# Optimization experiments

Measured on AMD Instinct MI355X. Metric: run time of the kernel, lower is better.

Reference implementation:

```python
import jax, jax.numpy as jnp
import numpy as np

B, C, T, H = 256, 8, 1024, 512
WB_INC = 0.05  # task_data_generator.wb_inc


def setup_inputs() -> dict:
    key = jax.random.key(0)
    ks = jax.random.split(key, 8)
    # arms/time strictly positive to keep the likelihood division well-conditioned
    inputs = jax.random.uniform(ks[0], (B, C, T), dtype=jnp.float32) + 0.5
    w_in = jax.random.normal(ks[1], (H, 6), dtype=jnp.float32) / np.sqrt(6.0).astype(np.float32)
    b_in = jax.random.normal(ks[2], (H,), dtype=jnp.float32) * 0.01
    w_rec = jax.random.normal(ks[3], (H, H), dtype=jnp.float32) / np.sqrt(float(H)).astype(np.float32)
    b_rec = jax.random.normal(ks[4], (H,), dtype=jnp.float32) * 0.01
    w_key = jax.random.normal(ks[5], (2, H), dtype=jnp.float32) / np.sqrt(float(H)).astype(np.float32)
    b_key = jax.random.normal(ks[6], (2,), dtype=jnp.float32) * 0.01
    # pre-drawn standard normals for the data-dependent noise injection (one per batch per step)
    z = jax.random.normal(ks[7], (T - 1, B), dtype=jnp.float32)
    return {"inputs": inputs, "w_in": w_in, "b_in": b_in, "w_rec": w_rec,
            "b_rec": b_rec, "w_key": w_key, "b_key": b_key, "z": z}


def _likelihood(tm, arms):
    # ((tm - arm) / (0.15*arm))^2, zeroed where tm == 0
    prs = ((tm[:, None] - arms) / (0.15 * arms)) ** 2
    return jnp.where(tm[:, None] == 0.0, 0.0, prs)


def _forward(inputs, w_in, b_in, w_rec, b_rec, w_key, b_key, z):
    Bsz, _, Tn = inputs.shape
    Hn = w_rec.shape[0]
    in_arms = inputs[:, :6, :]
    tm1 = inputs[:, 6, :]  # (B, T), never modified
    tm2 = inputs[:, 7, :]  # (B, T), receives cumulative noise offsets
    idx_tm1 = jnp.argmax(tm1, axis=1)          # (B,)
    ts = jnp.arange(1, Tn)
    tm1_done = ts[:, None] > idx_tm1[None, :]  # (T-1, B)
    arms_pri = jnp.moveaxis(in_arms[:, :2, 1:], 2, 0)  # (T-1, B, 2)
    arms_sec = jnp.moveaxis(in_arms[:, 2:, 1:], 2, 0)  # (T-1, B, 4)
    tm1_seq = tm1[:, 1:].T                              # (T-1, B)
    tm2_seq = tm2[:, 1:].T                              # (T-1, B)

    def step(carry, xs):
        h_pre, key_h_pre, side_h_pre, offset = carry
        ap, asec, t1, t2o, done, zt = xs
        side_h = key_h_pre > 0.5
        arms_sum = asec[:, :2] * key_h_pre[:, None] + asec[:, 2:] * (1.0 - key_h_pre)[:, None]
        closer1 = jnp.argmin(jnp.abs(ap - t1[:, None]), axis=1) == 0
        away = side_h != closer1
        switched = (side_h != side_h_pre) & done & away
        # in-place suffix update in_time[b,1,t:] += N(0, |wb_inc*tm2_t|) == cumulative per-batch offset
        t2_cur = t2o + offset
        offset = offset + jnp.where(switched, zt * jnp.abs(WB_INC * t2_cur), 0.0)
        t2_eff = t2o + offset
        pr1 = _likelihood(t1, ap)
        pr2 = _likelihood(t2_eff, arms_sum)
        prs_t = jnp.concatenate([pr1, pr2], axis=1)          # (B, 4)
        inp_t = jnp.concatenate([ap, arms_sum, t1[:, None], t2_eff[:, None]], axis=1)  # (B, 6)
        h_t = jnp.tanh(inp_t @ w_in.T + b_in + h_pre @ w_rec.T + b_rec)
        key_t = jax.nn.sigmoid(h_t @ w_key.T + b_key)        # (B, 2)
        return (h_t, key_t[:, 0], side_h, offset), (h_t, prs_t, key_t, t2_eff)

    carry0 = (jnp.zeros((Bsz, Hn), dtype=inputs.dtype),
              jnp.ones((Bsz,), dtype=inputs.dtype),
              jnp.ones((Bsz,), dtype=bool),
              jnp.zeros((Bsz,), dtype=inputs.dtype))
    _, (hs_s, prs_s, keys_s, tm2_s) = jax.lax.scan(
        step, carry0, (arms_pri, arms_sec, tm1_seq, tm2_seq, tm1_done, z))
    # loop starts at t=1; t=0 slots stay zero
    hs = jnp.concatenate([jnp.zeros((Bsz, Hn, 1), dtype=inputs.dtype), jnp.moveaxis(hs_s, 0, 2)], axis=2)
    prs = jnp.concatenate([jnp.zeros((Bsz, 4, 1), dtype=inputs.dtype), jnp.moveaxis(prs_s, 0, 2)], axis=2)
    keys = jnp.concatenate([jnp.zeros((Bsz, 2, 1), dtype=inputs.dtype), jnp.moveaxis(keys_s, 0, 2)], axis=2)
    tm2_mod = jnp.concatenate([tm2[:, :1], tm2_s.T], axis=1)
    tm_modified = jnp.stack([tm1, tm2_mod], axis=1)  # (B, 2, T)
    return keys, prs, hs, tm_modified


def reference(inputs, w_in, b_in, w_rec, b_rec, w_key, b_key, z):
    return _forward(inputs, w_in, b_in, w_rec, b_rec, w_key, b_key, z)
```

## Files before the change

kernel.cpp:

```cpp
#include <hip/hip_runtime.h>
#include <math.h>

#define TN 1024
#define HH 512
#define BB 256
#define NTHR 512
#define NW48 48
#define TSTRIDE 136

#define OFF_KEYS 0L
#define OFF_PRS  524288L
#define OFF_HS   1572864L
#define OFF_TM   135790592L

typedef float f32x4 __attribute__((ext_vector_type(4)));
typedef _Float16 f16x2 __attribute__((ext_vector_type(2)));

__device__ __forceinline__ float sigm(float x) { return 1.0f / (1.0f + expf(-x)); }

__device__ __forceinline__ float dot2(unsigned a, unsigned b, float c) {
#if __has_builtin(__builtin_amdgcn_fdot2)
    return __builtin_amdgcn_fdot2(__builtin_bit_cast(f16x2, a),
                                  __builtin_bit_cast(f16x2, b), c, false);
#else
    const f16x2 x = __builtin_bit_cast(f16x2, a);
    const f16x2 y = __builtin_bit_cast(f16x2, b);
    return fmaf((float)x.y, (float)y.y, fmaf((float)x.x, (float)y.x, c));
#endif
}

__global__ __launch_bounds__(256) void conv_fp16(const float* __restrict__ w,
                                                 _Float16* __restrict__ o) {
    const int i = (blockIdx.x * 256 + threadIdx.x) * 4;
    const f32x4 v = *(const f32x4*)(w + i);
    _Float16 r[4];
    #pragma unroll
    for (int k = 0; k < 4; ++k) r[k] = (_Float16)v[k];
    *(unsigned long long*)(o + i) = *(const unsigned long long*)r;
}

__global__ __launch_bounds__(NTHR, 2) void rnn_fused(
    const float* __restrict__ in, const float* __restrict__ w_in,
    const float* __restrict__ b_in, const float* __restrict__ b_rec,
    const float* __restrict__ w_key, const float* __restrict__ b_key,
    const float* __restrict__ z, float* __restrict__ out,
    const _Float16* __restrict__ whf)
{
    __shared__ __align__(16) _Float16 wtail[HH][TSTRIDE];
    __shared__ __align__(16) float tbuf[HH][9];
    __shared__ __align__(16) _Float16 hsh[2][HH];
    __shared__ float keysT[2][2][16];
    __shared__ float prsT[2][4][16];
    __shared__ float tmT[2][16];
    __shared__ float inp6[8];
    __shared__ float kred[8][2];

    const int tid = threadIdx.x;
    const int bb  = blockIdx.x;
    const int wv  = tid >> 6, ln = tid & 63;
    const float* inb = in + (long)bb * 8 * TN;
    const unsigned* wrow = (const unsigned*)(whf + (long)tid * HH);

    uint4 wreg[NW48];
    #pragma unroll
    for (int i = 0; i < NW48; ++i) wreg[i] = *(const uint4*)(wrow + i * 4);
    {
        const uint4* src = (const uint4*)(wrow + 192);
        #pragma unroll
        for (int i = 0; i < 16; ++i) *(uint4*)&wtail[tid][i * 8] = src[i];
    }

    const float bs  = b_in[tid] + b_rec[tid];
    const float wk0 = w_key[tid], wk1 = w_key[HH + tid];
    const float* wip = w_in + tid * 6;
    const float wi0 = wip[0], wi1 = wip[1], wi2 = wip[2];
    const float wi3 = wip[3], wi4 = wip[4], wi5 = wip[5];

    hsh[0][tid] = (_Float16)0.0f;
    tbuf[tid][0] = 0.0f;
    if (tid < 256) {
        f32x4 v = *(const f32x4*)(inb + 6 * TN + tid * 4);
        __builtin_nontemporal_store(v, (f32x4*)(out + OFF_TM + (long)bb * 2 * TN + tid * 4));
    }
    if (tid == 0) {
        keysT[0][0][0] = 0.f; keysT[0][1][0] = 0.f;
        prsT[0][0][0] = 0.f; prsT[0][1][0] = 0.f;
        prsT[0][2][0] = 0.f; prsT[0][3][0] = 0.f;
        tmT[0][0] = inb[7 * TN];
    }
    int idxm = 0;
    if (wv == 0) {
        const float* tp = inb + 6 * TN;
        float bv = -3.0e38f; int bi = 0;
        for (int i = 0; i < 16; ++i) { int tt = i * 64 + ln; float v = tp[tt]; if (v > bv) { bv = v; bi = tt; } }
        #pragma unroll
        for (int m = 1; m < 64; m <<= 1) {
            float ov = __shfl_xor(bv, m); int oi = __shfl_xor(bi, m);
            if (ov > bv || (ov == bv && oi < bi)) { bv = ov; bi = oi; }
        }
        idxm = bi;
    }
    float kh = 1.0f, off = 0.0f; int side_pre = 1;
    float q0=0,q1=0,q2=0,q3=0,q4=0,q5=0,q6=0,q7=0,qz=0;
    const float bk0 = b_key[0], bk1 = b_key[1];
    if (tid == 0) {
        q0=inb[1]; q1=inb[TN+1]; q2=inb[2*TN+1]; q3=inb[3*TN+1];
        q4=inb[4*TN+1]; q5=inb[5*TN+1]; q6=inb[6*TN+1]; q7=inb[7*TN+1];
        qz=z[bb];
    }
    __syncthreads();

    for (int t = 1; t < TN; ++t) {
        const int par1 = (t - 1) & 1, par2 = t & 1;
        const int tile = (t >> 4) & 1, sl = t & 15;

        if (tid == 0) {
            if (t > 1) {
                float k0 = 0.f, k1 = 0.f;
                #pragma unroll
                for (int w = 0; w < 8; ++w) { k0 += kred[w][0]; k1 += kred[w][1]; }
                const float key0 = sigm(k0 + bk0), key1 = sigm(k1 + bk1);
                const int pt = t - 1;
                keysT[(pt >> 4) & 1][0][pt & 15] = key0;
                keysT[(pt >> 4) & 1][1][pt & 15] = key1;
                kh = key0;
            }
            const int side = (kh > 0.5f);
            const float as0 = q2 * kh + q4 * (1.0f - kh);
            const float as1 = q3 * kh + q5 * (1.0f - kh);
            const int closer1 = (fabsf(q0 - q6) <= fabsf(q1 - q6));
            const int done = (t > idxm);
            const int sw = ((side != side_pre) && done && (side != closer1));
            const float t2c = q7 + off;
            if (sw) off += qz * fabsf(0.05f * t2c);
            const float t2e = q7 + off;
            side_pre = side;
            float u0 = (q6 - q0) / (0.15f * q0);    float pr10 = (q6 == 0.f) ? 0.f : u0 * u0;
            float u1 = (q6 - q1) / (0.15f * q1);    float pr11 = (q6 == 0.f) ? 0.f : u1 * u1;
            float u2 = (t2e - as0) / (0.15f * as0); float pr20 = (t2e == 0.f) ? 0.f : u2 * u2;
            float u3 = (t2e - as1) / (0.15f * as1); float pr21 = (t2e == 0.f) ? 0.f : u3 * u3;
            prsT[tile][0][sl] = pr10; prsT[tile][1][sl] = pr11;
            prsT[tile][2][sl] = pr20; prsT[tile][3][sl] = pr21;
            tmT[tile][sl] = t2e;
            inp6[0] = q0; inp6[1] = q1; inp6[2] = as0;
            inp6[3] = as1; inp6[4] = q6; inp6[5] = t2e;
            const int tn = (t < TN - 1) ? t + 1 : t;
            q0 = inb[tn]; q1 = inb[TN + tn]; q2 = inb[2 * TN + tn]; q3 = inb[3 * TN + tn];
            q4 = inb[4 * TN + tn]; q5 = inb[5 * TN + tn]; q6 = inb[6 * TN + tn]; q7 = inb[7 * TN + tn];
            qz = z[(long)(tn - 1) * BB + bb];
        }

        float a0 = 0.f, a1 = 0.f, a2 = 0.f, a3 = 0.f;
        const unsigned* hb = (const unsigned*)&hsh[par1][0];
        #pragma unroll
        for (int i = 0; i < NW48; ++i) {
            const uint4 hu = *(const uint4*)(hb + i * 4);
            a0 = dot2(wreg[i].x, hu.x, a0);
            a1 = dot2(wreg[i].y, hu.y, a1);
            a2 = dot2(wreg[i].z, hu.z, a2);
            a3 = dot2(wreg[i].w, hu.w, a3);
        }
        #pragma unroll
        for (int i = 0; i < 16; ++i) {
            const uint4 hu = *(const uint4*)(hb + 192 + i * 4);
            const uint4 wu = *(const uint4*)&wtail[tid][i * 8];
            a0 = dot2(wu.x, hu.x, a0);
            a1 = dot2(wu.y, hu.y, a1);
            a2 = dot2(wu.z, hu.z, a2);
            a3 = dot2(wu.w, hu.w, a3);
        }
        const float sdot = (a0 + a1) + (a2 + a3);
        __syncthreads();

        {
            const float s = sdot + bs
                          + wi0 * inp6[0] + wi1 * inp6[1] + wi2 * inp6[2]
                          + wi3 * inp6[3] + wi4 * inp6[4] + wi5 * inp6[5];
            const float h = tanhf(s);
            hsh[par2][tid] = (_Float16)h;
            tbuf[tid][t & 7] = h;
            float ka0 = h * wk0, ka1 = h * wk1;
            #pragma unroll
            for (int m = 1; m < 64; m <<= 1) { ka0 += __shfl_xor(ka0, m); ka1 += __shfl_xor(ka1, m); }
            if (ln == 0) { kred[wv][0] = ka0; kred[wv][1] = ka1; }
        }
        __syncthreads();

        if ((t & 7) == 7) {
            const int t0 = t - 7;
            const float* tr = &tbuf[tid][0];
            f32x4 v0, v1;
            v0.x = tr[0]; v0.y = tr[1]; v0.z = tr[2]; v0.w = tr[3];
            v1.x = tr[4]; v1.y = tr[5]; v1.z = tr[6]; v1.w = tr[7];
            float* dst = out + OFF_HS + ((long)bb * HH + tid) * TN + t0;
            __builtin_nontemporal_store(v0, (f32x4*)dst);
            __builtin_nontemporal_store(v1, (f32x4*)(dst + 4));
        }
        if ((t & 15) == 0 && wv == 0) {
            const int f = tile ^ 1, t0 = t - 16;
            if (ln < 8) {
                const int ch = ln >> 2, c4 = ln & 3;
                __builtin_nontemporal_store(*(const f32x4*)&keysT[f][ch][c4 * 4],
                    (f32x4*)(out + OFF_KEYS + (long)bb * 2 * TN + ch * TN + t0 + c4 * 4));
            } else if (ln < 24) {
                const int ix = ln - 8, ch = ix >> 2, c4 = ix & 3;
                __builtin_nontemporal_store(*(const f32x4*)&prsT[f][ch][c4 * 4],
                    (f32x4*)(out + OFF_PRS + (long)bb * 4 * TN + ch * TN + t0 + c4 * 4));
            } else if (ln < 28) {
                const int c4 = ln - 24;
                __builtin_nontemporal_store(*(const f32x4*)&tmT[f][c4 * 4],
                    (f32x4*)(out + OFF_TM + (long)bb * 2 * TN + TN + t0 + c4 * 4));
            }
        }
    }

    if (tid == 0) {
        float k0 = 0.f, k1 = 0.f;
        #pragma unroll
        for (int w = 0; w < 8; ++w) { k0 += kred[w][0]; k1 += kred[w][1]; }
        keysT[1][0][15] = sigm(k0 + bk0);
        keysT[1][1][15] = sigm(k1 + bk1);
    }
    __syncthreads();
    if (wv == 0) {
        const int f = 1, t0 = TN - 16;
        if (ln < 8) {
            const int ch = ln >> 2, c4 = ln & 3;
            __builtin_nontemporal_store(*(const f32x4*)&keysT[f][ch][c4 * 4],
                (f32x4*)(out + OFF_KEYS + (long)bb * 2 * TN + ch * TN + t0 + c4 * 4));
        } else if (ln < 24) {
            const int ix = ln - 8, ch = ix >> 2, c4 = ix & 3;
            __builtin_nontemporal_store(*(const f32x4*)&prsT[f][ch][c4 * 4],
                (f32x4*)(out + OFF_PRS + (long)bb * 4 * TN + ch * TN + t0 + c4 * 4));
        } else if (ln < 28) {
            const int c4 = ln - 24;
            __builtin_nontemporal_store(*(const f32x4*)&tmT[f][c4 * 4],
                (f32x4*)(out + OFF_TM + (long)bb * 2 * TN + TN + t0 + c4 * 4));
        }
    }
}

extern "C" void kernel_launch(void* const* d_in, const int* in_sizes, int n_in,
                              void* d_out, int out_size, void* d_ws, size_t ws_size,
                              hipStream_t stream) {
    (void)in_sizes; (void)n_in; (void)out_size; (void)ws_size;
    const float* in    = (const float*)d_in[0];
    const float* w_in  = (const float*)d_in[1];
    const float* b_in  = (const float*)d_in[2];
    const float* w_rec = (const float*)d_in[3];
    const float* b_rec = (const float*)d_in[4];
    const float* w_key = (const float*)d_in[5];
    const float* b_key = (const float*)d_in[6];
    const float* z     = (const float*)d_in[7];
    float* out = (float*)d_out;
    _Float16* whf = (_Float16*)d_ws;

    hipLaunchKernelGGL(conv_fp16, dim3(HH * HH / 1024), dim3(256), 0, stream, w_rec, whf);
    hipLaunchKernelGGL(rnn_fused, dim3(BB), dim3(NTHR), 0, stream,
                       in, w_in, b_in, b_rec, w_key, b_key, z, out, whf);
}
```

Measured before the change: 3.787 ms.

## Split each hidden row's dot product across two threads with 1024-thread blocks

Each block now runs 1024 threads, with two threads per hidden row. Each thread handles half of the 512-wide recurrent dot product, keeping 48 words of weights in registers and 24 in LDS, and reading the remaining 56 from global/L2 every step. The upper half writes its partial sums to shared memory, and the lower half combines them with the bias, tanh and key reduction. The upper half also takes over input prefetching and the output stores, with hidden-state tiles double-buffered so stores overlap the next step. The goal is to shorten the per-step serial dot-product latency, at the cost of an extra shared-memory combine, repeated global weight reads each step, and possibly lower occupancy from the larger block.

```diff
diff --git a/kernel.cpp b/kernel.cpp
--- a/kernel.cpp
+++ b/kernel.cpp
@@ -4,9 +4,7 @@
 #define TN 1024
 #define HH 512
 #define BB 256
-#define NTHR 512
-#define NW48 48
-#define TSTRIDE 136
+#define NTHR 1024
 
 #define OFF_KEYS 0L
 #define OFF_PRS  524288L
@@ -39,45 +37,53 @@
     *(unsigned long long*)(o + i) = *(const unsigned long long*)r;
 }
 
-__global__ __launch_bounds__(NTHR, 2) void rnn_fused(
+__global__
+__attribute__((amdgpu_flat_work_group_size(NTHR, NTHR), amdgpu_waves_per_eu(4, 4)))
+void rnn_fused(
     const float* __restrict__ in, const float* __restrict__ w_in,
     const float* __restrict__ b_in, const float* __restrict__ b_rec,
     const float* __restrict__ w_key, const float* __restrict__ b_key,
     const float* __restrict__ z, float* __restrict__ out,
     const _Float16* __restrict__ whf)
 {
-    __shared__ __align__(16) _Float16 wtail[HH][TSTRIDE];
-    __shared__ __align__(16) float tbuf[HH][9];
+    __shared__ __align__(16) unsigned wtail[NTHR][28];
+    __shared__ __align__(16) float tbuf[2][HH][9];
     __shared__ __align__(16) _Float16 hsh[2][HH];
+    __shared__ __align__(16) float pbuf[HH];
     __shared__ float keysT[2][2][16];
     __shared__ float prsT[2][4][16];
     __shared__ float tmT[2][16];
     __shared__ float inp6[8];
     __shared__ float kred[8][2];
 
-    const int tid = threadIdx.x;
-    const int bb  = blockIdx.x;
-    const int wv  = tid >> 6, ln = tid & 63;
+    const int tid  = threadIdx.x;
+    const int bb   = blockIdx.x;
+    const int wv   = tid >> 6, ln = tid & 63;
+    const int row  = tid & (HH - 1);
+    const int half = tid >> 9;
     const float* inb = in + (long)bb * 8 * TN;
-    const unsigned* wrow = (const unsigned*)(whf + (long)tid * HH);
-
-    uint4 wreg[NW48];
-    #pragma unroll
-    for (int i = 0; i < NW48; ++i) wreg[i] = *(const uint4*)(wrow + i * 4);
-    {
-        const uint4* src = (const uint4*)(wrow + 192);
-        #pragma unroll
-        for (int i = 0; i < 16; ++i) *(uint4*)&wtail[tid][i * 8] = src[i];
-    }
-
-    const float bs  = b_in[tid] + b_rec[tid];
-    const float wk0 = w_key[tid], wk1 = w_key[HH + tid];
-    const float* wip = w_in + tid * 6;
-    const float wi0 = wip[0], wi1 = wip[1], wi2 = wip[2];
-    const float wi3 = wip[3], wi4 = wip[4], wi5 = wip[5];
-
-    hsh[0][tid] = (_Float16)0.0f;
-    tbuf[tid][0] = 0.0f;
+    const unsigned* wseg = (const unsigned*)whf + (long)row * 256 + half * 128;
+
+    unsigned wreg[48];
+    #pragma unroll
+    for (int j = 0; j < 12; ++j) {
+        const uint4 v = *(const uint4*)(wseg + j * 4);
+        wreg[j * 4 + 0] = v.x; wreg[j * 4 + 1] = v.y;
+        wreg[j * 4 + 2] = v.z; wreg[j * 4 + 3] = v.w;
+    }
+    #pragma unroll
+    for (int i = 0; i < 48; ++i) asm volatile("" : "+v"(wreg[i]));
+
+    #pragma unroll
+    for (int j = 0; j < 6; ++j)
+        *(uint4*)&wtail[tid][j * 4] = *(const uint4*)(wseg + 48 + j * 4);
+
+    const float bs  = b_in[row] + b_rec[row];
+    const float wk0 = w_key[row], wk1 = w_key[HH + row];
+    const float wi0 = w_in[row * 6 + 0], wi1 = w_in[row * 6 + 1], wi2 = w_in[row * 6 + 2];
+    const float wi3 = w_in[row * 6 + 3], wi4 = w_in[row * 6 + 4], wi5 = w_in[row * 6 + 5];
+
+    if (tid < HH) { hsh[0][tid] = (_Float16)0.0f; tbuf[0][tid][0] = 0.0f; }
     if (tid < 256) {
         f32x4 v = *(const f32x4*)(inb + 6 * TN + tid * 4);
         __builtin_nontemporal_store(v, (f32x4*)(out + OFF_TM + (long)bb * 2 * TN + tid * 4));
@@ -89,7 +95,7 @@
         tmT[0][0] = inb[7 * TN];
     }
     int idxm = 0;
-    if (wv == 0) {
+    if (wv == 8) {
         const float* tp = inb + 6 * TN;
         float bv = -3.0e38f; int bi = 0;
         for (int i = 0; i < 16; ++i) { int tt = i * 64 + ln; float v = tp[tt]; if (v > bv) { bv = v; bi = tt; } }
@@ -101,20 +107,21 @@
         idxm = bi;
     }
     float kh = 1.0f, off = 0.0f; int side_pre = 1;
-    float q0=0,q1=0,q2=0,q3=0,q4=0,q5=0,q6=0,q7=0,qz=0;
+    float q0 = 0, q1 = 0, q2 = 0, q3 = 0, q4 = 0, q5 = 0, q6 = 0, q7 = 0, qz = 0;
     const float bk0 = b_key[0], bk1 = b_key[1];
-    if (tid == 0) {
-        q0=inb[1]; q1=inb[TN+1]; q2=inb[2*TN+1]; q3=inb[3*TN+1];
-        q4=inb[4*TN+1]; q5=inb[5*TN+1]; q6=inb[6*TN+1]; q7=inb[7*TN+1];
-        qz=z[bb];
+    if (tid == 512) {
+        q0 = inb[1]; q1 = inb[TN + 1]; q2 = inb[2 * TN + 1]; q3 = inb[3 * TN + 1];
+        q4 = inb[4 * TN + 1]; q5 = inb[5 * TN + 1]; q6 = inb[6 * TN + 1]; q7 = inb[7 * TN + 1];
+        qz = z[bb];
     }
     __syncthreads();
 
     for (int t = 1; t < TN; ++t) {
         const int par1 = (t - 1) & 1, par2 = t & 1;
         const int tile = (t >> 4) & 1, sl = t & 15;
-
-        if (tid == 0) {
+        const int tb8  = (t >> 3) & 1;
+
+        if (tid == 512) {
             if (t > 1) {
                 float k0 = 0.f, k1 = 0.f;
                 #pragma unroll
@@ -144,60 +151,102 @@
             tmT[tile][sl] = t2e;
             inp6[0] = q0; inp6[1] = q1; inp6[2] = as0;
             inp6[3] = as1; inp6[4] = q6; inp6[5] = t2e;
-            const int tn = (t < TN - 1) ? t + 1 : t;
-            q0 = inb[tn]; q1 = inb[TN + tn]; q2 = inb[2 * TN + tn]; q3 = inb[3 * TN + tn];
-            q4 = inb[4 * TN + tn]; q5 = inb[5 * TN + tn]; q6 = inb[6 * TN + tn]; q7 = inb[7 * TN + tn];
-            qz = z[(long)(tn - 1) * BB + bb];
         }
 
         float a0 = 0.f, a1 = 0.f, a2 = 0.f, a3 = 0.f;
-        const unsigned* hb = (const unsigned*)&hsh[par1][0];
-        #pragma unroll
-        for (int i = 0; i < NW48; ++i) {
-            const uint4 hu = *(const uint4*)(hb + i * 4);
-            a0 = dot2(wreg[i].x, hu.x, a0);
-            a1 = dot2(wreg[i].y, hu.y, a1);
-            a2 = dot2(wreg[i].z, hu.z, a2);
-            a3 = dot2(wreg[i].w, hu.w, a3);
-        }
-        #pragma unroll
-        for (int i = 0; i < 16; ++i) {
-            const uint4 hu = *(const uint4*)(hb + 192 + i * 4);
-            const uint4 wu = *(const uint4*)&wtail[tid][i * 8];
-            a0 = dot2(wu.x, hu.x, a0);
-            a1 = dot2(wu.y, hu.y, a1);
-            a2 = dot2(wu.z, hu.z, a2);
-            a3 = dot2(wu.w, hu.w, a3);
-        }
-        const float sdot = (a0 + a1) + (a2 + a3);
+        const unsigned* hbase = (const unsigned*)&hsh[par1][half * 256];
+        #pragma unroll
+        for (int j = 0; j < 14; ++j) {
+            const uint4 wu = *(const uint4*)(wseg + 72 + j * 4);
+            const uint4 hu = *(const uint4*)(hbase + 72 + j * 4);
+            a0 = dot2(wu.x, hu.x, a0); a1 = dot2(wu.y, hu.y, a1);
+            a2 = dot2(wu.z, hu.z, a2); a3 = dot2(wu.w, hu.w, a3);
+        }
+        #pragma unroll
+        for (int j = 0; j < 12; ++j) {
+            const uint4 hu = *(const uint4*)(hbase + j * 4);
+            a0 = dot2(wreg[j * 4 + 0], hu.x, a0); a1 = dot2(wreg[j * 4 + 1], hu.y, a1);
+            a2 = dot2(wreg[j * 4 + 2], hu.z, a2); a3 = dot2(wreg[j * 4 + 3], hu.w, a3);
+        }
+        #pragma unroll
+        for (int j = 0; j < 6; ++j) {
+            const uint4 wu = *(const uint4*)&wtail[tid][j * 4];
+            const uint4 hu = *(const uint4*)(hbase + 48 + j * 4);
+            a0 = dot2(wu.x, hu.x, a0); a1 = dot2(wu.y, hu.y, a1);
+            a2 = dot2(wu.z, hu.z, a2); a3 = dot2(wu.w, hu.w, a3);
+        }
+        const float part = (a0 + a1) + (a2 + a3);
+        if (tid >= HH) pbuf[row] = part;
         __syncthreads();
 
-        {
-            const float s = sdot + bs
+        if (tid < HH) {
+            const float s = part + pbuf[tid] + bs
                           + wi0 * inp6[0] + wi1 * inp6[1] + wi2 * inp6[2]
                           + wi3 * inp6[3] + wi4 * inp6[4] + wi5 * inp6[5];
             const float h = tanhf(s);
             hsh[par2][tid] = (_Float16)h;
-            tbuf[tid][t & 7] = h;
+            tbuf[tb8][tid][t & 7] = h;
             float ka0 = h * wk0, ka1 = h * wk1;
             #pragma unroll
             for (int m = 1; m < 64; m <<= 1) { ka0 += __shfl_xor(ka0, m); ka1 += __shfl_xor(ka1, m); }
             if (ln == 0) { kred[wv][0] = ka0; kred[wv][1] = ka1; }
+        } else {
+            if (tid == 512) {
+                const int tn = (t < TN - 1) ? t + 1 : t;
+                q0 = inb[tn]; q1 = inb[TN + tn]; q2 = inb[2 * TN + tn]; q3 = inb[3 * TN + tn];
+                q4 = inb[4 * TN + tn]; q5 = inb[5 * TN + tn]; q6 = inb[6 * TN + tn]; q7 = inb[7 * TN + tn];
+                qz = z[(long)(tn - 1) * BB + bb];
+            }
+            if ((t & 7) == 0) {
+                const int fb = tb8 ^ 1, t0 = t - 8;
+                const float* tr = &tbuf[fb][row][0];
+                f32x4 v0, v1;
+                v0.x = tr[0]; v0.y = tr[1]; v0.z = tr[2]; v0.w = tr[3];
+                v1.x = tr[4]; v1.y = tr[5]; v1.z = tr[6]; v1.w = tr[7];
+                float* dst = out + OFF_HS + ((long)bb * HH + row) * TN + t0;
+                __builtin_nontemporal_store(v0, (f32x4*)dst);
+                __builtin_nontemporal_store(v1, (f32x4*)(dst + 4));
+            }
+            if ((t & 15) == 0 && wv == 8) {
+                const int f = tile ^ 1, t0 = t - 16;
+                if (ln < 8) {
+                    const int ch = ln >> 2, c4 = ln & 3;
+                    __builtin_nontemporal_store(*(const f32x4*)&keysT[f][ch][c4 * 4],
+                        (f32x4*)(out + OFF_KEYS + (long)bb * 2 * TN + ch * TN + t0 + c4 * 4));
+                } else if (ln < 24) {
+                    const int ix = ln - 8, ch = ix >> 2, c4 = ix & 3;
+                    __builtin_nontemporal_store(*(const f32x4*)&prsT[f][ch][c4 * 4],
+                        (f32x4*)(out + OFF_PRS + (long)bb * 4 * TN + ch * TN + t0 + c4 * 4));
+                } else if (ln < 28) {
+                    const int c4 = ln - 24;
+                    __builtin_nontemporal_store(*(const f32x4*)&tmT[f][c4 * 4],
+                        (f32x4*)(out + OFF_TM + (long)bb * 2 * TN + TN + t0 + c4 * 4));
+                }
+            }
         }
         __syncthreads();
-
-        if ((t & 7) == 7) {
-            const int t0 = t - 7;
-            const float* tr = &tbuf[tid][0];
+    }
+
+    if (tid == 512) {
+        float k0 = 0.f, k1 = 0.f;
+        #pragma unroll
+        for (int w = 0; w < 8; ++w) { k0 += kred[w][0]; k1 += kred[w][1]; }
+        keysT[1][0][15] = sigm(k0 + bk0);
+        keysT[1][1][15] = sigm(k1 + bk1);
+    }
+    __syncthreads();
+    if (tid >= HH) {
+        {
+            const float* tr = &tbuf[1][row][0];
             f32x4 v0, v1;
             v0.x = tr[0]; v0.y = tr[1]; v0.z = tr[2]; v0.w = tr[3];
             v1.x = tr[4]; v1.y = tr[5]; v1.z = tr[6]; v1.w = tr[7];
-            float* dst = out + OFF_HS + ((long)bb * HH + tid) * TN + t0;
+            float* dst = out + OFF_HS + ((long)bb * HH + row) * TN + (TN - 8);
             __builtin_nontemporal_store(v0, (f32x4*)dst);
             __builtin_nontemporal_store(v1, (f32x4*)(dst + 4));
         }
-        if ((t & 15) == 0 && wv == 0) {
-            const int f = tile ^ 1, t0 = t - 16;
+        if (wv == 8) {
+            const int f = 1, t0 = TN - 16;
             if (ln < 8) {
                 const int ch = ln >> 2, c4 = ln & 3;
                 __builtin_nontemporal_store(*(const f32x4*)&keysT[f][ch][c4 * 4],
@@ -211,31 +260,6 @@
                 __builtin_nontemporal_store(*(const f32x4*)&tmT[f][c4 * 4],
                     (f32x4*)(out + OFF_TM + (long)bb * 2 * TN + TN + t0 + c4 * 4));
             }
-        }
-    }
-
-    if (tid == 0) {
-        float k0 = 0.f, k1 = 0.f;
-        #pragma unroll
-        for (int w = 0; w < 8; ++w) { k0 += kred[w][0]; k1 += kred[w][1]; }
-        keysT[1][0][15] = sigm(k0 + bk0);
-        keysT[1][1][15] = sigm(k1 + bk1);
-    }
-    __syncthreads();
-    if (wv == 0) {
-        const int f = 1, t0 = TN - 16;
-        if (ln < 8) {
-            const int ch = ln >> 2, c4 = ln & 3;
-            __builtin_nontemporal_store(*(const f32x4*)&keysT[f][ch][c4 * 4],
-                (f32x4*)(out + OFF_KEYS + (long)bb * 2 * TN + ch * TN + t0 + c4 * 4));
-        } else if (ln < 24) {
-            const int ix = ln - 8, ch = ix >> 2, c4 = ix & 3;
-            __builtin_nontemporal_store(*(const f32x4*)&prsT[f][ch][c4 * 4],
-                (f32x4*)(out + OFF_PRS + (long)bb * 4 * TN + ch * TN + t0 + c4 * 4));
-        } else if (ln < 28) {
-            const int c4 = ln - 24;
-            __builtin_nontemporal_store(*(const f32x4*)&tmT[f][c4 * 4],
-                (f32x4*)(out + OFF_TM + (long)bb * 2 * TN + TN + t0 + c4 * 4));
         }
     }
 }
```

Result: slower. 3.900 ms (+3.0%).
